# Optimization experiments

Measured on AMD Instinct MI355X. Metric: run time of the kernel, lower is better.

The kernel has to match this reference:

```python
import jax, jax.numpy as jnp
import numpy as np

B, T, C_IN, DIM, NFFT, HOP = 8, 1024, 256, 512, 1024, 256
NOUT = NFFT // 2 + 1
BB_DIL = (1, 1, 2, 2, 4, 4, 8, 8)
RES_DIL = (1, 3, 5)
N_RES = 3


def conv1d(x, w, b, dilation=1, groups=1, padding=0):
    # x: (B,C,T), w: (O, I/groups, K)
    y = jax.lax.conv_general_dilated(
        x, w, window_strides=(1,), padding=[(padding, padding)],
        rhs_dilation=(dilation,), dimension_numbers=('NCH', 'OIH', 'NCH'),
        feature_group_count=groups)
    return y + b[None, :, None]


def layernorm(x, g, b, eps=1e-6):
    m = jnp.mean(x, -1, keepdims=True)
    v = jnp.mean((x - m) ** 2, -1, keepdims=True)
    return (x - m) * jax.lax.rsqrt(v + eps) * g + b


def istft(spec, window):
    # spec: (B, F, Tf) complex, center=True, hann window, win_length=n_fft
    Bsz, F_, Tf = spec.shape
    frames = jnp.fft.irfft(spec, n=NFFT, axis=1)            # (B, n_fft, Tf)
    frames = jnp.transpose(frames, (0, 2, 1)) * window       # (B, Tf, n_fft)
    L = NFFT + HOP * (Tf - 1)
    idx = jnp.arange(Tf)[:, None] * HOP + jnp.arange(NFFT)[None, :]  # (Tf, n_fft)
    y = jnp.zeros((Bsz, L), frames.dtype).at[:, idx].add(frames)
    env = jnp.zeros((L,), window.dtype).at[idx].add(
        jnp.broadcast_to(window ** 2, (Tf, NFFT)))
    y = y / jnp.where(env > 1e-11, env, 1.0)
    start = NFFT // 2
    return y[:, start:start + HOP * (Tf - 1)]


def setup_inputs() -> dict:
    key = jax.random.key(0)
    ks = iter(jax.random.split(key, 64))
    r = lambda *s: jax.random.normal(next(ks), s, jnp.float32) * 0.02
    return {
        'x': jax.random.normal(next(ks), (B, T, C_IN), jnp.float32),
        'conv_in_w': r(DIM, C_IN, 7), 'conv_in_b': r(DIM),
        'skip_w': r(DIM, C_IN, 1), 'skip_b': r(DIM),
        'bb_dw_w': r(8, DIM, 1, 7), 'bb_dw_b': r(8, DIM),
        'bb_ln_g': jnp.ones((8, DIM), jnp.float32), 'bb_ln_b': jnp.zeros((8, DIM), jnp.float32),
        'bb_pw1_w': r(8, 4 * DIM, DIM), 'bb_pw1_b': r(8, 4 * DIM),
        'bb_pw2_w': r(8, DIM, 4 * DIM), 'bb_pw2_b': r(8, DIM),
        'bb_gamma': jnp.full((8, DIM), 1e-6, jnp.float32),
        'res_w1': r(N_RES, 3, DIM, DIM, 3), 'res_b1': r(N_RES, 3, DIM),
        'res_w2': r(N_RES, 3, DIM, DIM, 3), 'res_b2': r(N_RES, 3, DIM),
        'ln_g': jnp.ones((DIM,), jnp.float32), 'ln_b': jnp.zeros((DIM,), jnp.float32),
        'mag_w1': r(DIM, DIM), 'mag_b1': r(DIM),
        'mag_w2': r(NOUT, DIM), 'mag_b2': r(NOUT),
        'ph_w': r(NOUT, DIM), 'ph_b': r(NOUT),
        'cumsum_w': jnp.linspace(0.05, 0.4, NOUT, dtype=jnp.float32)[None, :],
        'window': (0.5 - 0.5 * jnp.cos(2.0 * jnp.pi * jnp.arange(NFFT) / NFFT)).astype(jnp.float32),
    }


def reference(x, conv_in_w, conv_in_b, skip_w, skip_b,
              bb_dw_w, bb_dw_b, bb_ln_g, bb_ln_b,
              bb_pw1_w, bb_pw1_b, bb_pw2_w, bb_pw2_b, bb_gamma,
              res_w1, res_b1, res_w2, res_b2,
              ln_g, ln_b, mag_w1, mag_b1, mag_w2, mag_b2,
              ph_w, ph_b, cumsum_w, window):
    # (B,T,C) -> (B,C,T)
    h = jnp.transpose(x, (0, 2, 1))
    skip = conv1d(h, skip_w, skip_b)                     # (B,DIM,T)
    hp = jnp.pad(h, ((0, 0), (0, 0), (3, 3)), mode='reflect')
    h = conv1d(hp, conv_in_w, conv_in_b)                 # kernel 7, pad 0 -> (B,DIM,T)
    # ConvNeXt backbone
    for i, d in enumerate(BB_DIL):
        res = h
        pad = (7 + (d - 1) * 6) // 2
        y = conv1d(h, bb_dw_w[i], bb_dw_b[i], dilation=d, groups=DIM, padding=pad)
        y = jnp.transpose(y, (0, 2, 1))                  # (B,T,DIM)
        y = layernorm(y, bb_ln_g[i], bb_ln_b[i])
        y = jax.nn.gelu(y @ bb_pw1_w[i].T + bb_pw1_b[i], approximate=False)
        y = y @ bb_pw2_w[i].T + bb_pw2_b[i]
        y = bb_gamma[i] * y
        h = res + jnp.transpose(y, (0, 2, 1))
    h = h + skip                                         # same length T
    # Residual dilated conv stacks
    for i in range(N_RES):
        for j, d in enumerate(RES_DIL):
            y = conv1d(h, res_w1[i, j], res_b1[i, j], dilation=d, padding=d)
            y = jax.nn.leaky_relu(y, 0.1)
            y = conv1d(y, res_w2[i, j], res_b2[i, j], padding=1)
            h = h + y
    h = jnp.transpose(h, (0, 2, 1))                      # (B,T,DIM)
    h = layernorm(h, ln_g, ln_b)
    # magnitude head
    m = jax.nn.gelu(h @ mag_w1.T + mag_b1, approximate=False)
    log_mag = m @ mag_w2.T + mag_b2
    mag = jnp.exp(jnp.clip(log_mag, -10.0, 10.0))        # (B,T,NOUT)
    # instantaneous-frequency phase head
    inst = jnp.tanh(h @ ph_w.T + ph_b) * jnp.pi
    phase = jnp.cumsum(inst * cumsum_w, axis=1)
    phase = jnp.remainder(phase + jnp.pi, 2.0 * jnp.pi) - jnp.pi
    # synthesize
    spec = jax.lax.complex(mag * jnp.cos(phase), mag * jnp.sin(phase))
    spec = jnp.transpose(spec, (0, 2, 1))                # (B,F,T)
    return istft(spec, window)
```

## Files before the change

### kernel.cpp

```cpp
#include <hip/hip_runtime.h>
#include <math.h>

constexpr int Bv = 8, Tv = 1024, DIMC = 512, NOUTC = 513;
constexpr int Mrows = Bv * 1024;
constexpr int LDS_S = 1056;
constexpr float PI_F = 3.14159265358979323846f;
constexpr float TWOPI_F = 6.28318530717958647692f;

struct TapInfo { int n; int off[7]; };
struct PtrTable { _Float16* h[36]; };

enum { BND_NONE = 0, BND_ZERO, BND_REFLECT };

typedef _Float16 half8v __attribute__((ext_vector_type(8)));
typedef _Float16 half4v __attribute__((ext_vector_type(4)));
typedef float f32x4 __attribute__((ext_vector_type(4)));

__device__ __forceinline__ void gld_lds16(const void* g, void* l) {
  __builtin_amdgcn_global_load_lds(
      (const __attribute__((address_space(1))) unsigned int*)g,
      (__attribute__((address_space(3))) unsigned int*)l, 16, 0, 0);
}

enum { MEPI_GELU_H = 0, MEPI_GAMMARES };

template<int EPI, int TN>
__global__ __launch_bounds__(256)
void mfma_gemm(const _Float16* __restrict__ A, int lda,
               const _Float16* __restrict__ W, int K,
               const float* __restrict__ bias,
               const float* __restrict__ aux,
               float* __restrict__ hio,
               _Float16* __restrict__ Ch,
               int N, int ldc)
{
  constexpr int NFR = TN / 32;
  __shared__ _Float16 sA[2][128 * 32];
  __shared__ _Float16 sB[2][TN * 32];
  const int m0 = blockIdx.x * 128;
  const int n0 = blockIdx.y * TN;
  const int tid = threadIdx.x;
  const int wid = tid >> 6, lane = tid & 63;
  const int wr = wid >> 1, wc = wid & 1;
  const int fr = lane & 15, fq = lane >> 4;

  f32x4 acc[4][NFR] = {};

  const int rbase = tid >> 2;
  const int kwS = (((tid & 3) ^ ((tid >> 3) & 3)) << 3);
  const int nkc = K >> 5;
  const int fqS = fq ^ ((fr >> 1) & 3);
  const int aBase = (wr * 64 + fr) * 32 + fqS * 8;
  const int bBase = (wc * (TN / 2) + fr) * 32 + fqS * 8;

  const _Float16* arow[2];
  #pragma unroll
  for (int s = 0; s < 2; ++s)
    arow[s] = A + (size_t)(m0 + s * 64 + rbase) * lda + kwS;

  auto STAGE = [&](int kc, int buf) {
    const int k0 = kc << 5;
    #pragma unroll
    for (int s = 0; s < 2; ++s)
      gld_lds16(arow[s] + k0, (char*)&sA[buf][0] + s * 4096 + wid * 1024);
    #pragma unroll
    for (int s = 0; s < TN / 64; ++s) {
      size_t bo = (size_t)(n0 + s * 64 + rbase) * K + kwS + k0;
      gld_lds16(W + bo, (char*)&sB[buf][0] + s * 4096 + wid * 1024);
    }
  };
  auto COMPUTE = [&](int buf) {
    half8v aF[4], bF[NFR];
    #pragma unroll
    for (int i = 0; i < 4; ++i) aF[i] = *(const half8v*)&sA[buf][aBase + i * 512];
    #pragma unroll
    for (int j = 0; j < NFR; ++j) bF[j] = *(const half8v*)&sB[buf][bBase + j * 512];
    #pragma unroll
    for (int i = 0; i < 4; ++i)
      #pragma unroll
      for (int j = 0; j < NFR; ++j)
        acc[i][j] = __builtin_amdgcn_mfma_f32_16x16x32_f16(aF[i], bF[j], acc[i][j], 0, 0, 0);
  };

  STAGE(0, 0);
  __syncthreads();
  int cur = 0;
  for (int kc = 0; kc < nkc; ++kc) {
    if (kc + 1 < nkc) STAGE(kc + 1, cur ^ 1);
    COMPUTE(cur);
    __syncthreads();
    cur ^= 1;
  }

  #pragma unroll
  for (int j = 0; j < NFR; ++j) {
    const int n = n0 + wc * (TN / 2) + j * 16 + fr;
    const float bj = bias[n];
    const float gj = (EPI == MEPI_GAMMARES) ? aux[n] : 0.f;
    #pragma unroll
    for (int i = 0; i < 4; ++i) {
      const int mB = m0 + wr * 64 + i * 16 + fq * 4;
      #pragma unroll
      for (int r = 0; r < 4; ++r) {
        const int m = mB + r;
        float v = acc[i][j][r] + bj;
        if (EPI == MEPI_GELU_H) {
          v = 0.5f * v * (1.f + erff(v * 0.70710678118654752f));
          Ch[(size_t)m * ldc + n] = (_Float16)v;
        } else {
          hio[(size_t)m * ldc + n] += gj * v;
        }
      }
    }
  }
}

enum { SEPI_F32 = 0, SEPI_LEAKY_SPLIT, SEPI_ADDRES_SPLIT,
       SEPI_GELU_SPLIT, SEPI_EXPCLIP, SEPI_TANHCW };

template<int EPI, int BND, int TN>
__global__ __launch_bounds__(256)
void mfma_gemm_split(const _Float16* __restrict__ Ah, const _Float16* __restrict__ Al, int lda,
                     const _Float16* __restrict__ Wh, const _Float16* __restrict__ Wl, int K,
                     const float* __restrict__ bias,
                     const float* __restrict__ aux,
                     float* __restrict__ hio,
                     float* __restrict__ Cf,
                     _Float16* __restrict__ Chh, _Float16* __restrict__ Chl,
                     int N, int ldc,
                     const _Float16* __restrict__ zpage,
                     TapInfo taps)
{
  constexpr int NFR = TN / 32;
  __shared__ _Float16 sAh[2][128 * 32];
  __shared__ _Float16 sAl[2][128 * 32];
  __shared__ _Float16 sBh[2][TN * 32];
  __shared__ _Float16 sBl[2][TN * 32];
  const int m0 = blockIdx.x * 128;
  const int n0 = blockIdx.y * TN;
  const int tid = threadIdx.x;
  const int wid = tid >> 6, lane = tid & 63;
  const int wr = wid >> 1, wc = wid & 1;
  const int fr = lane & 15, fq = lane >> 4;

  f32x4 acc[4][NFR] = {};

  const int t0 = m0 & (Tv - 1);
  const int rbase = tid >> 2;
  const int kwS = (((tid & 3) ^ ((tid >> 3) & 3)) << 3);
  const int nkc = K >> 5;
  const int NT = taps.n * nkc;
  const int fqS = fq ^ ((fr >> 1) & 3);
  const int aBase = (wr * 64 + fr) * 32 + fqS * 8;
  const int bBase = (wc * (TN / 2) + fr) * 32 + fqS * 8;

  auto STAGE = [&](int st, int buf) {
    int tap = (taps.n == 1) ? 0 : (st / nkc);
    int kc = st - tap * nkc;
    const int k0 = kc << 5;
    const int off = (BND == BND_NONE) ? 0 : taps.off[tap];
    const _Float16* Wth = Wh + (size_t)tap * N * K;
    const _Float16* Wtl = Wl + (size_t)tap * N * K;
    #pragma unroll
    for (int s = 0; s < 2; ++s) {
      int t = t0 + s * 64 + rbase + off;
      bool valid = true;
      if (BND == BND_REFLECT) t = (t < 0) ? -t : (t >= Tv ? 2 * Tv - 2 - t : t);
      else if (BND == BND_ZERO) valid = (t >= 0) && (t < Tv);
      size_t ro = (size_t)(m0 - t0 + t) * lda + kwS + k0;
      const void* sh = valid ? (const void*)(Ah + ro) : (const void*)zpage;
      const void* sl = valid ? (const void*)(Al + ro) : (const void*)zpage;
      gld_lds16(sh, (char*)&sAh[buf][0] + s * 4096 + wid * 1024);
      gld_lds16(sl, (char*)&sAl[buf][0] + s * 4096 + wid * 1024);
    }
    #pragma unroll
    for (int s = 0; s < TN / 64; ++s) {
      size_t bo = (size_t)(n0 + s * 64 + rbase) * K + kwS + k0;
      gld_lds16(Wth + bo, (char*)&sBh[buf][0] + s * 4096 + wid * 1024);
      gld_lds16(Wtl + bo, (char*)&sBl[buf][0] + s * 4096 + wid * 1024);
    }
  };

  auto COMPUTE = [&](int buf) {
    half8v ah[4], al[4], bh[NFR], bl[NFR];
    #pragma unroll
    for (int i = 0; i < 4; ++i) {
      ah[i] = *(const half8v*)&sAh[buf][aBase + i * 512];
      al[i] = *(const half8v*)&sAl[buf][aBase + i * 512];
    }
    #pragma unroll
    for (int j = 0; j < NFR; ++j) {
      bh[j] = *(const half8v*)&sBh[buf][bBase + j * 512];
      bl[j] = *(const half8v*)&sBl[buf][bBase + j * 512];
    }
    #pragma unroll
    for (int i = 0; i < 4; ++i)
      #pragma unroll
      for (int j = 0; j < NFR; ++j) {
        acc[i][j] = __builtin_amdgcn_mfma_f32_16x16x32_f16(ah[i], bh[j], acc[i][j], 0, 0, 0);
        acc[i][j] = __builtin_amdgcn_mfma_f32_16x16x32_f16(ah[i], bl[j], acc[i][j], 0, 0, 0);
        acc[i][j] = __builtin_amdgcn_mfma_f32_16x16x32_f16(al[i], bh[j], acc[i][j], 0, 0, 0);
      }
  };

  STAGE(0, 0);
  __syncthreads();
  int cur = 0;
  for (int st = 0; st < NT; ++st) {
    if (st + 1 < NT) STAGE(st + 1, cur ^ 1);
    COMPUTE(cur);
    __syncthreads();
    cur ^= 1;
  }

  #pragma unroll
  for (int j = 0; j < NFR; ++j) {
    const int n = n0 + wc * (TN / 2) + j * 16 + fr;
    const bool nok = (n < N);
    const float bj = (nok && bias) ? bias[n] : 0.f;
    const float ax = (EPI == SEPI_TANHCW && nok) ? aux[n] : 0.f;
    #pragma unroll
    for (int i = 0; i < 4; ++i) {
      const int mB = m0 + wr * 64 + i * 16 + fq * 4;
      #pragma unroll
      for (int r = 0; r < 4; ++r) {
        const int m = mB + r;
        float v = acc[i][j][r] + bj;
        if (!nok) continue;
        if (EPI == SEPI_F32) {
          Cf[(size_t)m * ldc + n] = v;
        } else if (EPI == SEPI_GELU_SPLIT) {
          v = 0.5f * v * (1.f + erff(v * 0.70710678118654752f));
          _Float16 hi = (_Float16)v;
          Chh[(size_t)m * ldc + n] = hi;
          Chl[(size_t)m * ldc + n] = (_Float16)(v - (float)hi);
        } else if (EPI == SEPI_EXPCLIP) {
          Cf[(size_t)m * ldc + n] = expf(fminf(fmaxf(v, -10.f), 10.f));
        } else if (EPI == SEPI_TANHCW) {
          Cf[(size_t)m * ldc + n] = tanhf(v) * PI_F * ax;
        }
      }
    }
  }
}

enum { REPI_LEAKY = 0, REPI_ADDRES };

template<int EPI>
__global__ __launch_bounds__(256)
void res_gemm(const _Float16* __restrict__ Ah, const _Float16* __restrict__ Al,
              const _Float16* __restrict__ Wh, const _Float16* __restrict__ Wl,
              const float* __restrict__ bias,
              float* __restrict__ hio,
              _Float16* __restrict__ Chh, _Float16* __restrict__ Chl,
              const _Float16* __restrict__ zpage,
              int d)
{
  __shared__ _Float16 sAh_[160 * 32];
  __shared__ _Float16 sAl_[160 * 32];
  __shared__ _Float16 sB_[3 * 2 * 64 * 32];
  const int m0 = blockIdx.x * 128;
  const int n0 = blockIdx.y * 64;
  const int tid = threadIdx.x;
  const int wid = tid >> 6, lane = tid & 63;
  const int wr = wid >> 1, wc = wid & 1;
  const int fr = lane & 15, fq = lane >> 4;
  const int t0 = m0 & (Tv - 1);

  f32x4 acc[4][2] = {};
  const int offs[3] = {-d, 0, d};

  for (int kc = 0; kc < 16; ++kc) {
    const int k0h = kc << 5;
    #pragma unroll
    for (int it = 0; it < 5; ++it) {
      int cb = it * 4 + wid;
      int half = (cb >= 10) ? 1 : 0;
      int rb = (cb - half * 10) * 16;
      int row = rb + (lane >> 2);
      int slot_g = (lane & 3) ^ ((row >> 1) & 3);
      int t = t0 - 16 + row;
      bool valid = (t >= 0) && (t < Tv);
      const _Float16* srcb = half ? Al : Ah;
      const void* src = valid
          ? (const void*)(srcb + (size_t)(m0 - t0 + t) * DIMC + k0h + slot_g * 8)
          : (const void*)(zpage + slot_g * 8);
      void* dst = (char*)(half ? sAl_ : sAh_) + rb * 64;
      gld_lds16(src, dst);
    }
    #pragma unroll
    for (int it = 0; it < 6; ++it) {
      int cb = it * 4 + wid;
      int tap = cb >> 3;
      int r2 = cb & 7;
      int half = r2 >> 2;
      int rb = (r2 & 3) * 16;
      int row = rb + (lane >> 2);
      int slot_g = (lane & 3) ^ ((row >> 1) & 3);
      const _Float16* srcb = (half ? Wl : Wh) + (size_t)tap * 512 * 512
                           + (size_t)(n0 + row) * 512 + k0h + slot_g * 8;
      void* dst = (char*)sB_ + ((size_t)(tap * 2 + half) * 64 + rb) * 64;
      gld_lds16(srcb, dst);
    }
    __syncthreads();

    #pragma unroll
    for (int tap = 0; tap < 3; ++tap) {
      const int off = offs[tap];
      half8v ah[4], al[4], bh[2], bl[2];
      #pragma unroll
      for (int i = 0; i < 4; ++i) {
        int rA = wr * 64 + i * 16 + fr + off + 16;
        int ab = rA * 64 + ((fq ^ ((rA >> 1) & 3)) * 16);
        ah[i] = *(const half8v*)((const char*)sAh_ + ab);
        al[i] = *(const half8v*)((const char*)sAl_ + ab);
      }
      #pragma unroll
      for (int j = 0; j < 2; ++j) {
        int rB = wc * 32 + j * 16 + fr;
        int bb = rB * 64 + ((fq ^ ((rB >> 1) & 3)) * 16);
        bh[j] = *(const half8v*)((const char*)sB_ + (tap * 2 + 0) * 4096 + bb);
        bl[j] = *(const half8v*)((const char*)sB_ + (tap * 2 + 1) * 4096 + bb);
      }
      #pragma unroll
      for (int i = 0; i < 4; ++i)
        #pragma unroll
        for (int j = 0; j < 2; ++j) {
          acc[i][j] = __builtin_amdgcn_mfma_f32_16x16x32_f16(ah[i], bh[j], acc[i][j], 0, 0, 0);
          acc[i][j] = __builtin_amdgcn_mfma_f32_16x16x32_f16(ah[i], bl[j], acc[i][j], 0, 0, 0);
          acc[i][j] = __builtin_amdgcn_mfma_f32_16x16x32_f16(al[i], bh[j], acc[i][j], 0, 0, 0);
        }
    }
    __syncthreads();
  }

  #pragma unroll
  for (int j = 0; j < 2; ++j) {
    const int n = n0 + wc * 32 + j * 16 + fr;
    const float bj = bias[n];
    #pragma unroll
    for (int i = 0; i < 4; ++i) {
      const int mB = m0 + wr * 64 + i * 16 + fq * 4;
      #pragma unroll
      for (int r = 0; r < 4; ++r) {
        const int m = mB + r;
        float v = acc[i][j][r] + bj;
        if (EPI == REPI_LEAKY) {
          v = (v > 0.f) ? v : 0.1f * v;
          _Float16 hi = (_Float16)v;
          Chh[(size_t)m * DIMC + n] = hi;
          Chl[(size_t)m * DIMC + n] = (_Float16)(v - (float)hi);
        } else {
          float nh = hio[(size_t)m * DIMC + n] + v;
          hio[(size_t)m * DIMC + n] = nh;
          _Float16 hi = (_Float16)nh;
          Chh[(size_t)m * DIMC + n] = hi;
          Chl[(size_t)m * DIMC + n] = (_Float16)(nh - (float)hi);
        }
      }
    }
  }
}

__global__ __launch_bounds__(256)
void convin_gemm(const _Float16* __restrict__ Ah, const _Float16* __restrict__ Al,
                 const _Float16* __restrict__ Wh, const _Float16* __restrict__ Wl,
                 const float* __restrict__ bias,
                 float* __restrict__ Cf)
{
  __shared__ _Float16 sAh_[160 * 32];
  __shared__ _Float16 sAl_[160 * 32];
  __shared__ _Float16 sB_[7 * 2 * 64 * 32];
  const int m0 = blockIdx.x * 128;
  const int n0 = blockIdx.y * 64;
  const int tid = threadIdx.x;
  const int wid = tid >> 6, lane = tid & 63;
  const int wr = wid >> 1, wc = wid & 1;
  const int fr = lane & 15, fq = lane >> 4;
  const int t0 = m0 & (Tv - 1);

  f32x4 acc[4][2] = {};

  for (int kc = 0; kc < 8; ++kc) {
    const int k0h = kc << 5;
    #pragma unroll
    for (int it = 0; it < 5; ++it) {
      int cb = it * 4 + wid;
      int half = (cb >= 10) ? 1 : 0;
      int rb = (cb - half * 10) * 16;
      int row = rb + (lane >> 2);
      int slot_g = (lane & 3) ^ ((row >> 1) & 3);
      int t = t0 - 16 + row;
      t = (t < 0) ? -t : (t >= Tv ? 2 * Tv - 2 - t : t);
      const _Float16* srcb = half ? Al : Ah;
      const void* src = srcb + (size_t)(m0 - t0 + t) * 256 + k0h + slot_g * 8;
      void* dst = (char*)(half ? sAl_ : sAh_) + rb * 64;
      gld_lds16(src, dst);
    }
    #pragma unroll
    for (int it = 0; it < 14; ++it) {
      int cb = it * 4 + wid;
      int tap = cb >> 3;
      int r2 = cb & 7;
      int half = r2 >> 2;
      int rb = (r2 & 3) * 16;
      int row = rb + (lane >> 2);
      int slot_g = (lane & 3) ^ ((row >> 1) & 3);
      const _Float16* srcb = (half ? Wl : Wh) + (size_t)tap * 512 * 256
                           + (size_t)(n0 + row) * 256 + k0h + slot_g * 8;
      void* dst = (char*)sB_ + ((size_t)(tap * 2 + half) * 64 + rb) * 64;
      gld_lds16(srcb, dst);
    }
    __syncthreads();

    #pragma unroll
    for (int tap = 0; tap < 7; ++tap) {
      const int off = tap - 3;
      half8v ah[4], al[4], bh[2], bl[2];
      #pragma unroll
      for (int i = 0; i < 4; ++i) {
        int rA = wr * 64 + i * 16 + fr + off + 16;
        int ab = rA * 64 + ((fq ^ ((rA >> 1) & 3)) * 16);
        ah[i] = *(const half8v*)((const char*)sAh_ + ab);
        al[i] = *(const half8v*)((const char*)sAl_ + ab);
      }
      #pragma unroll
      for (int j = 0; j < 2; ++j) {
        int rB = wc * 32 + j * 16 + fr;
        int bb = rB * 64 + ((fq ^ ((rB >> 1) & 3)) * 16);
        bh[j] = *(const half8v*)((const char*)sB_ + (tap * 2 + 0) * 4096 + bb);
        bl[j] = *(const half8v*)((const char*)sB_ + (tap * 2 + 1) * 4096 + bb);
      }
      #pragma unroll
      for (int i = 0; i < 4; ++i)
        #pragma unroll
        for (int j = 0; j < 2; ++j) {
          acc[i][j] = __builtin_amdgcn_mfma_f32_16x16x32_f16(ah[i], bh[j], acc[i][j], 0, 0, 0);
          acc[i][j] = __builtin_amdgcn_mfma_f32_16x16x32_f16(ah[i], bl[j], acc[i][j], 0, 0, 0);
          acc[i][j] = __builtin_amdgcn_mfma_f32_16x16x32_f16(al[i], bh[j], acc[i][j], 0, 0, 0);
        }
    }
    __syncthreads();
  }

  #pragma unroll
  for (int j = 0; j < 2; ++j) {
    const int n = n0 + wc * 32 + j * 16 + fr;
    const float bj = bias[n];
    #pragma unroll
    for (int i = 0; i < 4; ++i) {
      const int mB = m0 + wr * 64 + i * 16 + fq * 4;
      #pragma unroll
      for (int r = 0; r < 4; ++r) {
        const int m = mB + r;
        Cf[(size_t)m * DIMC + n] = acc[i][j][r] + bj;
      }
    }
  }
}

__global__ __launch_bounds__(256)
void dwln(const float* __restrict__ h, const float* __restrict__ wt,
          const float* __restrict__ bias, const float* __restrict__ g,
          const float* __restrict__ be, _Float16* __restrict__ out, int d)
{
  int wid = threadIdx.x >> 6, lane = threadIdx.x & 63;
  int m = (blockIdx.x << 2) + wid;
  int t = m & (Tv - 1);
  int bT = m - t;
  int c0 = lane * 8;
  float acc[8];
  {
    float4 b0 = *(const float4*)&bias[c0];
    float4 b1 = *(const float4*)&bias[c0 + 4];
    acc[0] = b0.x; acc[1] = b0.y; acc[2] = b0.z; acc[3] = b0.w;
    acc[4] = b1.x; acc[5] = b1.y; acc[6] = b1.z; acc[7] = b1.w;
  }
  #pragma unroll
  for (int k = 0; k < 7; ++k) {
    int tt = t + (k - 3) * d;
    if (tt < 0 || tt >= Tv) continue;
    const float* hp = &h[(size_t)(bT + tt) * DIMC + c0];
    float4 v0 = *(const float4*)hp;
    float4 v1 = *(const float4*)(hp + 4);
    const float* wp = &wt[k * DIMC + c0];
    float4 w0 = *(const float4*)wp;
    float4 w1 = *(const float4*)(wp + 4);
    float hv[8] = {v0.x, v0.y, v0.z, v0.w, v1.x, v1.y, v1.z, v1.w};
    float wv[8] = {w0.x, w0.y, w0.z, w0.w, w1.x, w1.y, w1.z, w1.w};
    #pragma unroll
    for (int q = 0; q < 8; ++q)
      acc[q] = fmaf(hv[q], wv[q], acc[q]);
  }
  float sum = 0.f;
  #pragma unroll
  for (int q = 0; q < 8; ++q) sum += acc[q];
  #pragma unroll
  for (int o = 32; o > 0; o >>= 1) sum += __shfl_xor(sum, o);
  float mean = sum * (1.f / 512.f);
  float vs = 0.f;
  #pragma unroll
  for (int q = 0; q < 8; ++q) { float dd = acc[q] - mean; vs = fmaf(dd, dd, vs); }
  #pragma unroll
  for (int o = 32; o > 0; o >>= 1) vs += __shfl_xor(vs, o);
  float rstd = rsqrtf(vs * (1.f / 512.f) + 1e-6f);
  float4 g0 = *(const float4*)&g[c0];
  float4 g1 = *(const float4*)&g[c0 + 4];
  float4 e0 = *(const float4*)&be[c0];
  float4 e1 = *(const float4*)&be[c0 + 4];
  float gv[8] = {g0.x, g0.y, g0.z, g0.w, g1.x, g1.y, g1.z, g1.w};
  float ev[8] = {e0.x, e0.y, e0.z, e0.w, e1.x, e1.y, e1.z, e1.w};
  half8v ov;
  #pragma unroll
  for (int q = 0; q < 8; ++q)
    ov[q] = (_Float16)((acc[q] - mean) * rstd * gv[q] + ev[q]);
  *(half8v*)&out[(size_t)m * DIMC + c0] = ov;
}

__global__ __launch_bounds__(256)
void repack_dw(const float* __restrict__ in, float* __restrict__ out)
{
  int idx = blockIdx.x * 256 + threadIdx.x;
  if (idx >= 8 * 512 * 7) return;
  int l = idx / 3584;
  int r = idx - l * 3584;
  int c = r / 7, k = r - c * 7;
  out[l * 3584 + k * 512 + c] = in[idx];
}

__global__ __launch_bounds__(256)
void lnorm_split(const float* __restrict__ in, const float* __restrict__ g,
                 const float* __restrict__ be,
                 _Float16* __restrict__ ohi, _Float16* __restrict__ olo)
{
  int wid = threadIdx.x >> 6, lane = threadIdx.x & 63;
  int m = (blockIdx.x << 2) + wid;
  int c0 = lane * 8;
  const float* row = in + (size_t)m * DIMC + c0;
  float4 v0 = *(const float4*)row;
  float4 v1 = *(const float4*)(row + 4);
  float acc[8] = {v0.x, v0.y, v0.z, v0.w, v1.x, v1.y, v1.z, v1.w};
  float sum = 0.f;
  #pragma unroll
  for (int q = 0; q < 8; ++q) sum += acc[q];
  #pragma unroll
  for (int o = 32; o > 0; o >>= 1) sum += __shfl_xor(sum, o);
  float mean = sum * (1.f / 512.f);
  float vs = 0.f;
  #pragma unroll
  for (int q = 0; q < 8; ++q) { float dd = acc[q] - mean; vs = fmaf(dd, dd, vs); }
  #pragma unroll
  for (int o = 32; o > 0; o >>= 1) vs += __shfl_xor(vs, o);
  float rstd = rsqrtf(vs * (1.f / 512.f) + 1e-6f);
  float4 g0 = *(const float4*)&g[c0];
  float4 g1 = *(const float4*)&g[c0 + 4];
  float4 e0 = *(const float4*)&be[c0];
  float4 e1 = *(const float4*)&be[c0 + 4];
  float gv[8] = {g0.x, g0.y, g0.z, g0.w, g1.x, g1.y, g1.z, g1.w};
  float ev[8] = {e0.x, e0.y, e0.z, e0.w, e1.x, e1.y, e1.z, e1.w};
  half8v hv, lv;
  #pragma unroll
  for (int q = 0; q < 8; ++q) {
    float v = (acc[q] - mean) * rstd * gv[q] + ev[q];
    _Float16 hi = (_Float16)v;
    hv[q] = hi; lv[q] = (_Float16)(v - (float)hi);
  }
  *(half8v*)&ohi[(size_t)m * DIMC + c0] = hv;
  *(half8v*)&olo[(size_t)m * DIMC + c0] = lv;
}

__global__ __launch_bounds__(256)
void add_split(float* __restrict__ a, const float* __restrict__ b,
               _Float16* __restrict__ hi, _Float16* __restrict__ lo, int n)
{
  int i = (blockIdx.x * 256 + threadIdx.x) * 4;
  if (i >= n) return;
  float4 va = *(const float4*)&a[i];
  float4 vb = *(const float4*)&b[i];
  float v[4] = {va.x + vb.x, va.y + vb.y, va.z + vb.z, va.w + vb.w};
  *(float4*)&a[i] = make_float4(v[0], v[1], v[2], v[3]);
  half4v h, l;
  #pragma unroll
  for (int q = 0; q < 4; ++q) {
    _Float16 hh = (_Float16)v[q];
    h[q] = hh; l[q] = (_Float16)(v[q] - (float)hh);
  }
  *(half4v*)&hi[i] = h;
  *(half4v*)&lo[i] = l;
}

__global__ __launch_bounds__(256)
void cvt_split(const float* __restrict__ in, _Float16* __restrict__ hi,
               _Float16* __restrict__ lo, int n)
{
  int i = (blockIdx.x * 256 + threadIdx.x) * 4;
  if (i >= n) return;
  float4 vv = *(const float4*)&in[i];
  float v[4] = {vv.x, vv.y, vv.z, vv.w};
  half4v h, l;
  #pragma unroll
  for (int q = 0; q < 4; ++q) {
    _Float16 hh = (_Float16)v[q];
    h[q] = hh; l[q] = (_Float16)(v[q] - (float)hh);
  }
  *(half4v*)&hi[i] = h;
  *(half4v*)&lo[i] = l;
}

__global__ __launch_bounds__(256)
void cvt_split_pad(const float* __restrict__ in, _Float16* __restrict__ hi,
                   _Float16* __restrict__ lo, int rows, int cols, int padRows)
{
  int i = blockIdx.x * 256 + threadIdx.x;
  if (i >= padRows * cols) return;
  int r = i / cols;
  float v = (r < rows) ? in[i] : 0.f;
  _Float16 h = (_Float16)v;
  hi[i] = h; lo[i] = (_Float16)(v - (float)h);
}

__global__ __launch_bounds__(256)
void cvt_h(const float* __restrict__ in, _Float16* __restrict__ out, int n)
{
  int i = (blockIdx.x * 256 + threadIdx.x) * 4;
  if (i >= n) return;
  float4 v = *(const float4*)&in[i];
  half4v h;
  h[0] = (_Float16)v.x; h[1] = (_Float16)v.y;
  h[2] = (_Float16)v.z; h[3] = (_Float16)v.w;
  *(half4v*)&out[i] = h;
}

__global__ __launch_bounds__(256)
void repack_split(const float* __restrict__ in, _Float16* __restrict__ hi,
                  _Float16* __restrict__ lo, int O, int C, int KT)
{
  int idx = blockIdx.x * 256 + threadIdx.x;
  if (idx >= O * C) return;
  int o = idx / C, c = idx - o * C;
  for (int k = 0; k < KT; ++k) {
    float v = in[((size_t)o * C + c) * KT + k];
    _Float16 h = (_Float16)v;
    size_t dst = ((size_t)k * O + o) * C + c;
    hi[dst] = h; lo[dst] = (_Float16)(v - (float)h);
  }
}

__global__ __launch_bounds__(256)
void repack_all(const float* __restrict__ res_w1, const float* __restrict__ res_w2,
                PtrTable pt)
{
  int blk = blockIdx.x;
  int conv = blk >> 10;
  int idx = ((blk & 1023) << 8) + threadIdx.x;
  int o = idx >> 9, c = idx & 511;
  const float* src = (conv < 9) ? (res_w1 + (size_t)conv * 786432)
                                : (res_w2 + (size_t)(conv - 9) * 786432);
  _Float16* hi = pt.h[conv * 2];
  _Float16* lo = pt.h[conv * 2 + 1];
  #pragma unroll
  for (int k = 0; k < 3; ++k) {
    float v = src[((size_t)o * 512 + c) * 3 + k];
    _Float16 hh = (_Float16)v;
    size_t dst = ((size_t)k * 512 + o) * 512 + c;
    hi[dst] = hh; lo[dst] = (_Float16)(v - (float)hh);
  }
}

__global__ __launch_bounds__(256)
void zero_fill16(_Float16* __restrict__ p)
{
  int i = threadIdx.x * 8;
  #pragma unroll
  for (int q = 0; q < 8; ++q) p[i + q] = (_Float16)0.f;
}

__global__ __launch_bounds__(256)
void build_basis_split(const float* __restrict__ window,
                       _Float16* __restrict__ bhi, _Float16* __restrict__ blo)
{
  int n = blockIdx.x;
  float wn = window[n];
  const float invN = 1.f / 1024.f;
  for (int j = threadIdx.x; j < LDS_S; j += 256) {
    float coef = 0.f;
    if (j < 513) {
      int k = j;
      if (k == 0)        coef = invN;
      else if (k == 512) coef = (n & 1) ? -invN : invN;
      else {
        int r = (k * n) & 1023;
        coef = 2.f * invN * cosf(TWOPI_F * (float)r * (1.f / 1024.f));
      }
    } else if (j < 1026) {
      int k = j - 513;
      if (k != 0 && k != 512) {
        int r = (k * n) & 1023;
        coef = -2.f * invN * sinf(TWOPI_F * (float)r * (1.f / 1024.f));
      }
    }
    float v = coef * wn;
    _Float16 hi = (_Float16)v;
    bhi[(size_t)n * LDS_S + j] = hi;
    blo[(size_t)n * LDS_S + j] = (_Float16)(v - (float)hi);
  }
}

__global__ __launch_bounds__(256)
void scan_part(const float* __restrict__ dph, float* __restrict__ psum)
{
  int b = blockIdx.x, fg = blockIdx.y;
  int w = threadIdx.x >> 6, lane = threadIdx.x & 63;
  int tc = blockIdx.z * 4 + w;
  int f = fg * 64 + lane;
  if (f >= NOUTC) return;
  const float* p = dph + (size_t)(b * Tv + tc * 32) * NOUTC + f;
  float s = 0.f;
  #pragma unroll 8
  for (int j = 0; j < 32; ++j) s += p[(size_t)j * NOUTC];
  psum[((size_t)b * 32 + tc) * 520 + f] = s;
}

__global__ __launch_bounds__(256)
void scan_off(float* __restrict__ psum)
{
  int idx = blockIdx.x * 256 + threadIdx.x;
  if (idx >= 8 * NOUTC) return;
  int b = idx / NOUTC, f = idx - b * NOUTC;
  float run = 0.f;
  for (int tc = 0; tc < 32; ++tc) {
    size_t o = ((size_t)b * 32 + tc) * 520 + f;
    float v = psum[o];
    psum[o] = run;
    run += v;
  }
}

__global__ __launch_bounds__(256)
void scan_emit(const float* __restrict__ dph, const float* __restrict__ mag,
               const float* __restrict__ psum,
               _Float16* __restrict__ Shi, _Float16* __restrict__ Slo)
{
  int b = blockIdx.x, fg = blockIdx.y;
  int w = threadIdx.x >> 6, lane = threadIdx.x & 63;
  int tc = blockIdx.z * 4 + w;
  int f = fg * 64 + lane;
  if (f >= NOUTC) return;
  float run = psum[((size_t)b * 32 + tc) * 520 + f];
  const size_t base = (size_t)(b * Tv + tc * 32) * NOUTC + f;
  for (int j = 0; j < 32; ++j) {
    run += dph[base + (size_t)j * NOUTC];
    float r = fmodf(run + PI_F, TWOPI_F);
    if (r < 0.f) r += TWOPI_F;
    float wph = r - PI_F;
    float mg = mag[base + (size_t)j * NOUTC];
    float sn, cs;
    sincosf(wph, &sn, &cs);
    size_t mrow = (size_t)(b * Tv + tc * 32 + j) * LDS_S;
    float vc = mg * cs, vs2 = mg * sn;
    _Float16 hc = (_Float16)vc, hs = (_Float16)vs2;
    Shi[mrow + f] = hc;        Slo[mrow + f] = (_Float16)(vc - (float)hc);
    Shi[mrow + 513 + f] = hs;  Slo[mrow + 513 + f] = (_Float16)(vs2 - (float)hs);
  }
}

__global__ __launch_bounds__(256)
void pad_S(_Float16* __restrict__ Shi, _Float16* __restrict__ Slo)
{
  int idx = blockIdx.x * 256 + threadIdx.x;
  if (idx >= Mrows * 30) return;
  int m = idx / 30, c = 1026 + idx % 30;
  Shi[(size_t)m * LDS_S + c] = (_Float16)0.f;
  Slo[(size_t)m * LDS_S + c] = (_Float16)0.f;
}

__global__ __launch_bounds__(256)
void ola(const float* __restrict__ frames, const float* __restrict__ window,
         float* __restrict__ out)
{
  int idx = blockIdx.x * 256 + threadIdx.x;
  if (idx >= Bv * 261888) return;
  int b = idx / 261888;
  int i = idx - b * 261888;
  int l = i + 512;
  int tmax = l >> 8; if (tmax > 1023) tmax = 1023;
  int tmin = (l >= 1023) ? ((l - 1023 + 255) >> 8) : 0;
  float acc = 0.f, env = 0.f;
  for (int t = tmin; t <= tmax; ++t) {
    int n = l - (t << 8);
    acc += frames[(size_t)(b * Tv + t) * 1024 + n];
    float wv = window[n];
    env = fmaf(wv, wv, env);
  }
  out[idx] = acc / (env > 1e-11f ? env : 1.f);
}

extern "C" void kernel_launch(void* const* d_in, const int* in_sizes, int n_in,
                              void* d_out, int out_size, void* d_ws, size_t ws_size,
                              hipStream_t stream)
{
  const float* x         = (const float*)d_in[0];
  const float* conv_in_w = (const float*)d_in[1];
  const float* conv_in_b = (const float*)d_in[2];
  const float* skip_w    = (const float*)d_in[3];
  const float* skip_b    = (const float*)d_in[4];
  const float* bb_dw_w   = (const float*)d_in[5];
  const float* bb_dw_b   = (const float*)d_in[6];
  const float* bb_ln_g   = (const float*)d_in[7];
  const float* bb_ln_b   = (const float*)d_in[8];
  const float* bb_pw1_w  = (const float*)d_in[9];
  const float* bb_pw1_b  = (const float*)d_in[10];
  const float* bb_pw2_w  = (const float*)d_in[11];
  const float* bb_pw2_b  = (const float*)d_in[12];
  const float* bb_gamma  = (const float*)d_in[13];
  const float* res_w1    = (const float*)d_in[14];
  const float* res_b1    = (const float*)d_in[15];
  const float* res_w2    = (const float*)d_in[16];
  const float* res_b2    = (const float*)d_in[17];
  const float* ln_g      = (const float*)d_in[18];
  const float* ln_b      = (const float*)d_in[19];
  const float* mag_w1    = (const float*)d_in[20];
  const float* mag_b1    = (const float*)d_in[21];
  const float* mag_w2    = (const float*)d_in[22];
  const float* mag_b2    = (const float*)d_in[23];
  const float* ph_w      = (const float*)d_in[24];
  const float* ph_b      = (const float*)d_in[25];
  const float* cumsum_w  = (const float*)d_in[26];
  const float* window    = (const float*)d_in[27];
  float* out = (float*)d_out;
  float* ws  = (float*)d_ws;

  float* w_h     = ws;
  float* w_skip  = ws + 4194304;
  float* w_t4    = ws + 8388608;
  float* w_mag   = ws + 12582912;
  float* w_dph   = ws + 16785408;
  float* w_basis = ws + 20987904;
  float* w_big   = ws + 22069248;
  _Float16* t3h  = (_Float16*)w_big;
  _Float16* h_hi = (_Float16*)w_big;
  _Float16* h_lo = h_hi + 4194304;
  _Float16* y_hi = h_hi + 8388608;
  _Float16* y_lo = h_hi + 12582912;
  _Float16* Shi  = (_Float16*)w_big;
  _Float16* Slo  = Shi + 8650752;
  float* w_frames= w_h;

  _Float16* t2h  = (_Float16*)(ws + 30720000);
  _Float16* x_hi = (_Float16*)(ws + 32817152);
  _Float16* x_lo = (_Float16*)(ws + 33865728);
  _Float16* wA_hi= (_Float16*)(ws + 34914304);
  _Float16* wA_lo= (_Float16*)(ws + 35438592);
  _Float16* wB_hi= (_Float16*)(ws + 35962880);
  _Float16* wB_lo= (_Float16*)(ws + 36487168);
  _Float16* zpg  = (_Float16*)(ws + 37011456);
  float* w_psum  = ws + 37012480;
  float* w_dwT   = ws + 37145600;

  _Float16* wpw1h = (_Float16*)w_t4;
  _Float16* wpw2h = (_Float16*)w_mag;

  static const size_t slotOffF[18] = {
    8388608, 9175040, 9961472, 10747904, 11534336,
    12582912, 13369344, 14155776, 14942208, 15728640,
    16785408, 17571840, 18358272, 19144704, 19931136,
    32817152, 33603584,
    30720000
  };
  PtrTable pt;
  for (int cv = 0; cv < 18; ++cv) {
    _Float16* hi = (_Float16*)(ws + slotOffF[cv]);
    pt.h[cv * 2] = hi;
    pt.h[cv * 2 + 1] = hi + 786432;
  }

  _Float16* lshi = (_Float16*)w_skip;
  _Float16* lslo = lshi + 4194304;
  _Float16* t4hi = (_Float16*)w_t4;
  _Float16* t4lo = t4hi + 4194304;
  _Float16* m1hi = t2h;
  _Float16* m1lo = t2h + 262144;
  _Float16* m2hi = t2h + 524288;
  _Float16* m2lo = t2h + 851968;
  _Float16* phhi = t2h + 1179648;
  _Float16* phlo = t2h + 1507328;
  _Float16* bhi  = (_Float16*)w_basis;
  _Float16* blo  = bhi + 1081344;

  dim3 blk(256);
  TapInfo tp1{1, {0}};

  zero_fill16<<<dim3(1), blk, 0, stream>>>(zpg);
  cvt_split<<<dim3(8192 * 256 / 4 / 256), blk, 0, stream>>>(x, x_hi, x_lo, 8192 * 256);
  cvt_h<<<dim3(8388608 / 4 / 256), blk, 0, stream>>>(bb_pw1_w, wpw1h, 8388608);
  cvt_h<<<dim3(8388608 / 4 / 256), blk, 0, stream>>>(bb_pw2_w, wpw2h, 8388608);
  repack_dw<<<dim3(112), blk, 0, stream>>>(bb_dw_w, w_dwT);

  repack_split<<<dim3(512 * 256 / 256), blk, 0, stream>>>(conv_in_w, wA_hi, wA_lo, 512, 256, 7);
  convin_gemm<<<dim3(64, 8), blk, 0, stream>>>(
      x_hi, x_lo, wA_hi, wA_lo, conv_in_b, w_h);
  repack_split<<<dim3(512 * 256 / 256), blk, 0, stream>>>(skip_w, wB_hi, wB_lo, 512, 256, 1);
  mfma_gemm_split<SEPI_F32, BND_NONE, 64><<<dim3(64, 8), blk, 0, stream>>>(
      x_hi, x_lo, 256, wB_hi, wB_lo, 256, skip_b, nullptr, nullptr, w_skip, nullptr, nullptr,
      512, 512, zpg, tp1);

  const int dil[8] = {1, 1, 2, 2, 4, 4, 8, 8};
  for (int i = 0; i < 8; ++i) {
    dwln<<<dim3(2048), blk, 0, stream>>>(w_h, w_dwT + i * 3584, bb_dw_b + i * 512,
                                         bb_ln_g + i * 512, bb_ln_b + i * 512, t2h, dil[i]);
    mfma_gemm<MEPI_GELU_H, 128><<<dim3(64, 16), blk, 0, stream>>>(
        t2h, 512, wpw1h + (size_t)i * 2048 * 512, 512, bb_pw1_b + i * 2048,
        nullptr, nullptr, t3h, 2048, 2048);
    mfma_gemm<MEPI_GAMMARES, 64><<<dim3(64, 8), blk, 0, stream>>>(
        t3h, 2048, wpw2h + (size_t)i * 512 * 2048, 2048, bb_pw2_b + i * 512,
        bb_gamma + i * 512, w_h, nullptr, 512, 512);
  }
  add_split<<<dim3(4194304 / 4 / 256), blk, 0, stream>>>(w_h, w_skip, h_hi, h_lo, 4194304);

  repack_all<<<dim3(18 * 1024), blk, 0, stream>>>(res_w1, res_w2, pt);

  const int rdil[3] = {1, 3, 5};
  for (int i = 0; i < 3; ++i)
    for (int j = 0; j < 3; ++j) {
      int d = rdil[j];
      int idx = i * 3 + j;
      res_gemm<REPI_LEAKY><<<dim3(64, 8), blk, 0, stream>>>(
          h_hi, h_lo, pt.h[idx * 2], pt.h[idx * 2 + 1],
          res_b1 + idx * 512, nullptr, y_hi, y_lo, zpg, d);
      res_gemm<REPI_ADDRES><<<dim3(64, 8), blk, 0, stream>>>(
          y_hi, y_lo, pt.h[(9 + idx) * 2], pt.h[(9 + idx) * 2 + 1],
          res_b2 + idx * 512, w_h, h_hi, h_lo, zpg, 1);
    }

  lnorm_split<<<dim3(2048), blk, 0, stream>>>(w_h, ln_g, ln_b, lshi, lslo);

  cvt_split<<<dim3(262144 / 4 / 256), blk, 0, stream>>>(mag_w1, m1hi, m1lo, 262144);
  cvt_split_pad<<<dim3(640 * 512 / 256), blk, 0, stream>>>(mag_w2, m2hi, m2lo, 513, 512, 640);
  cvt_split_pad<<<dim3(640 * 512 / 256), blk, 0, stream>>>(ph_w, phhi, phlo, 513, 512, 640);

  mfma_gemm_split<SEPI_GELU_SPLIT, BND_NONE, 64><<<dim3(64, 8), blk, 0, stream>>>(
      lshi, lslo, 512, m1hi, m1lo, 512, mag_b1, nullptr, nullptr, nullptr,
      t4hi, t4lo, 512, 512, zpg, tp1);
  mfma_gemm_split<SEPI_EXPCLIP, BND_NONE, 64><<<dim3(64, 10), blk, 0, stream>>>(
      t4hi, t4lo, 512, m2hi, m2lo, 512, mag_b2, nullptr, nullptr, w_mag,
      nullptr, nullptr, 513, 513, zpg, tp1);
  mfma_gemm_split<SEPI_TANHCW, BND_NONE, 64><<<dim3(64, 10), blk, 0, stream>>>(
      lshi, lslo, 512, phhi, phlo, 512, ph_b, cumsum_w, nullptr, w_dph,
      nullptr, nullptr, 513, 513, zpg, tp1);

  build_basis_split<<<dim3(1024), blk, 0, stream>>>(window, bhi, blo);
  pad_S<<<dim3((Mrows * 30 + 255) / 256), blk, 0, stream>>>(Shi, Slo);
  scan_part<<<dim3(8, 9, 8), blk, 0, stream>>>(w_dph, w_psum);
  scan_off<<<dim3(17), blk, 0, stream>>>(w_psum);
  scan_emit<<<dim3(8, 9, 8), blk, 0, stream>>>(w_dph, w_mag, w_psum, Shi, Slo);
  mfma_gemm_split<SEPI_F32, BND_NONE, 128><<<dim3(64, 8), blk, 0, stream>>>(
      Shi, Slo, LDS_S, bhi, blo, LDS_S, nullptr, nullptr, nullptr, w_frames,
      nullptr, nullptr, 1024, 1024, zpg, tp1);
  ola<<<dim3((Bv * 261888 + 255) / 256), blk, 0, stream>>>(w_frames, window, out);
}
```

Before: 1.865 ms.

## Widen res_gemm N tile to 128 and deepen K staging for pw2 GEMM

The residual dilated-conv GEMM now computes a 128-column output tile per block instead of 64. This halves the grid and reuses each staged A tile (hi/lo activations with halo) across twice as many output columns, cutting redundant A loads. The pointwise-2 backbone GEMM now stages two 32-wide K chunks per barrier, halving the synchronisation count over its K=2048 loop. In exchange, register pressure and LDS use rise, and res_gemm drops to 256 blocks, which lowers occupancy and parallelism on the GPU.

```diff
diff --git a/kernel.cpp b/kernel.cpp
--- a/kernel.cpp
+++ b/kernel.cpp
@@ -24,7 +24,7 @@
 
 enum { MEPI_GELU_H = 0, MEPI_GAMMARES };
 
-template<int EPI, int TN>
+template<int EPI, int TN, int KS>
 __global__ __launch_bounds__(256)
 void mfma_gemm(const _Float16* __restrict__ A, int lda,
                const _Float16* __restrict__ W, int K,
@@ -35,8 +35,8 @@
                int N, int ldc)
 {
   constexpr int NFR = TN / 32;
-  __shared__ _Float16 sA[2][128 * 32];
-  __shared__ _Float16 sB[2][TN * 32];
+  __shared__ _Float16 sA[2][KS * 128 * 32];
+  __shared__ _Float16 sB[2][KS * TN * 32];
   const int m0 = blockIdx.x * 128;
   const int n0 = blockIdx.y * TN;
   const int tid = threadIdx.x;
@@ -48,7 +48,7 @@
 
   const int rbase = tid >> 2;
   const int kwS = (((tid & 3) ^ ((tid >> 3) & 3)) << 3);
-  const int nkc = K >> 5;
+  const int nst = K / (32 * KS);
   const int fqS = fq ^ ((fr >> 1) & 3);
   const int aBase = (wr * 64 + fr) * 32 + fqS * 8;
   const int bBase = (wc * (TN / 2) + fr) * 32 + fqS * 8;
@@ -58,35 +58,45 @@
   for (int s = 0; s < 2; ++s)
     arow[s] = A + (size_t)(m0 + s * 64 + rbase) * lda + kwS;
 
-  auto STAGE = [&](int kc, int buf) {
-    const int k0 = kc << 5;
-    #pragma unroll
-    for (int s = 0; s < 2; ++s)
-      gld_lds16(arow[s] + k0, (char*)&sA[buf][0] + s * 4096 + wid * 1024);
-    #pragma unroll
-    for (int s = 0; s < TN / 64; ++s) {
-      size_t bo = (size_t)(n0 + s * 64 + rbase) * K + kwS + k0;
-      gld_lds16(W + bo, (char*)&sB[buf][0] + s * 4096 + wid * 1024);
+  auto STAGE = [&](int st, int buf) {
+    #pragma unroll
+    for (int ks = 0; ks < KS; ++ks) {
+      const int k0 = (st * KS + ks) << 5;
+      #pragma unroll
+      for (int s = 0; s < 2; ++s)
+        gld_lds16(arow[s] + k0,
+                  (char*)&sA[buf][0] + ks * 8192 + s * 4096 + wid * 1024);
+      #pragma unroll
+      for (int s = 0; s < TN / 64; ++s) {
+        size_t bo = (size_t)(n0 + s * 64 + rbase) * K + kwS + k0;
+        gld_lds16(W + bo,
+                  (char*)&sB[buf][0] + ks * (TN * 64) + s * 4096 + wid * 1024);
+      }
     }
   };
   auto COMPUTE = [&](int buf) {
-    half8v aF[4], bF[NFR];
-    #pragma unroll
-    for (int i = 0; i < 4; ++i) aF[i] = *(const half8v*)&sA[buf][aBase + i * 512];
-    #pragma unroll
-    for (int j = 0; j < NFR; ++j) bF[j] = *(const half8v*)&sB[buf][bBase + j * 512];
-    #pragma unroll
-    for (int i = 0; i < 4; ++i)
+    #pragma unroll
+    for (int ks = 0; ks < KS; ++ks) {
+      half8v aF[4], bF[NFR];
+      #pragma unroll
+      for (int i = 0; i < 4; ++i)
+        aF[i] = *(const half8v*)&sA[buf][ks * 4096 + aBase + i * 512];
       #pragma unroll
       for (int j = 0; j < NFR; ++j)
-        acc[i][j] = __builtin_amdgcn_mfma_f32_16x16x32_f16(aF[i], bF[j], acc[i][j], 0, 0, 0);
+        bF[j] = *(const half8v*)&sB[buf][ks * (TN * 32) + bBase + j * 512];
+      #pragma unroll
+      for (int i = 0; i < 4; ++i)
+        #pragma unroll
+        for (int j = 0; j < NFR; ++j)
+          acc[i][j] = __builtin_amdgcn_mfma_f32_16x16x32_f16(aF[i], bF[j], acc[i][j], 0, 0, 0);
+    }
   };
 
   STAGE(0, 0);
   __syncthreads();
   int cur = 0;
-  for (int kc = 0; kc < nkc; ++kc) {
-    if (kc + 1 < nkc) STAGE(kc + 1, cur ^ 1);
+  for (int st = 0; st < nst; ++st) {
+    if (st + 1 < nst) STAGE(st + 1, cur ^ 1);
     COMPUTE(cur);
     __syncthreads();
     cur ^= 1;
@@ -258,16 +268,16 @@
 {
   __shared__ _Float16 sAh_[160 * 32];
   __shared__ _Float16 sAl_[160 * 32];
-  __shared__ _Float16 sB_[3 * 2 * 64 * 32];
+  __shared__ _Float16 sB_[3 * 2 * 128 * 32];
   const int m0 = blockIdx.x * 128;
-  const int n0 = blockIdx.y * 64;
+  const int n0 = blockIdx.y * 128;
   const int tid = threadIdx.x;
   const int wid = tid >> 6, lane = tid & 63;
   const int wr = wid >> 1, wc = wid & 1;
   const int fr = lane & 15, fq = lane >> 4;
   const int t0 = m0 & (Tv - 1);
 
-  f32x4 acc[4][2] = {};
+  f32x4 acc[4][4] = {};
   const int offs[3] = {-d, 0, d};
 
   for (int kc = 0; kc < 16; ++kc) {
@@ -289,17 +299,17 @@
       gld_lds16(src, dst);
     }
     #pragma unroll
-    for (int it = 0; it < 6; ++it) {
+    for (int it = 0; it < 12; ++it) {
       int cb = it * 4 + wid;
-      int tap = cb >> 3;
-      int r2 = cb & 7;
-      int half = r2 >> 2;
-      int rb = (r2 & 3) * 16;
+      int tap = cb >> 4;
+      int r2 = cb & 15;
+      int half = r2 >> 3;
+      int rb = (r2 & 7) * 16;
       int row = rb + (lane >> 2);
       int slot_g = (lane & 3) ^ ((row >> 1) & 3);
       const _Float16* srcb = (half ? Wl : Wh) + (size_t)tap * 512 * 512
                            + (size_t)(n0 + row) * 512 + k0h + slot_g * 8;
-      void* dst = (char*)sB_ + ((size_t)(tap * 2 + half) * 64 + rb) * 64;
+      void* dst = (char*)sB_ + ((size_t)(tap * 2 + half) * 128 + rb) * 64;
       gld_lds16(srcb, dst);
     }
     __syncthreads();
@@ -307,7 +317,7 @@
     #pragma unroll
     for (int tap = 0; tap < 3; ++tap) {
       const int off = offs[tap];
-      half8v ah[4], al[4], bh[2], bl[2];
+      half8v ah[4], al[4], bh[4], bl[4];
       #pragma unroll
       for (int i = 0; i < 4; ++i) {
         int rA = wr * 64 + i * 16 + fr + off + 16;
@@ -316,16 +326,16 @@
         al[i] = *(const half8v*)((const char*)sAl_ + ab);
       }
       #pragma unroll
-      for (int j = 0; j < 2; ++j) {
-        int rB = wc * 32 + j * 16 + fr;
+      for (int j = 0; j < 4; ++j) {
+        int rB = wc * 64 + j * 16 + fr;
         int bb = rB * 64 + ((fq ^ ((rB >> 1) & 3)) * 16);
-        bh[j] = *(const half8v*)((const char*)sB_ + (tap * 2 + 0) * 4096 + bb);
-        bl[j] = *(const half8v*)((const char*)sB_ + (tap * 2 + 1) * 4096 + bb);
+        bh[j] = *(const half8v*)((const char*)sB_ + (tap * 2 + 0) * 8192 + bb);
+        bl[j] = *(const half8v*)((const char*)sB_ + (tap * 2 + 1) * 8192 + bb);
       }
       #pragma unroll
       for (int i = 0; i < 4; ++i)
         #pragma unroll
-        for (int j = 0; j < 2; ++j) {
+        for (int j = 0; j < 4; ++j) {
           acc[i][j] = __builtin_amdgcn_mfma_f32_16x16x32_f16(ah[i], bh[j], acc[i][j], 0, 0, 0);
           acc[i][j] = __builtin_amdgcn_mfma_f32_16x16x32_f16(ah[i], bl[j], acc[i][j], 0, 0, 0);
           acc[i][j] = __builtin_amdgcn_mfma_f32_16x16x32_f16(al[i], bh[j], acc[i][j], 0, 0, 0);
@@ -335,8 +345,8 @@
   }
 
   #pragma unroll
-  for (int j = 0; j < 2; ++j) {
-    const int n = n0 + wc * 32 + j * 16 + fr;
+  for (int j = 0; j < 4; ++j) {
+    const int n = n0 + wc * 64 + j * 16 + fr;
     const float bj = bias[n];
     #pragma unroll
     for (int i = 0; i < 4; ++i) {
@@ -908,10 +918,10 @@
   for (int i = 0; i < 8; ++i) {
     dwln<<<dim3(2048), blk, 0, stream>>>(w_h, w_dwT + i * 3584, bb_dw_b + i * 512,
                                          bb_ln_g + i * 512, bb_ln_b + i * 512, t2h, dil[i]);
-    mfma_gemm<MEPI_GELU_H, 128><<<dim3(64, 16), blk, 0, stream>>>(
+    mfma_gemm<MEPI_GELU_H, 128, 1><<<dim3(64, 16), blk, 0, stream>>>(
         t2h, 512, wpw1h + (size_t)i * 2048 * 512, 512, bb_pw1_b + i * 2048,
         nullptr, nullptr, t3h, 2048, 2048);
-    mfma_gemm<MEPI_GAMMARES, 64><<<dim3(64, 8), blk, 0, stream>>>(
+    mfma_gemm<MEPI_GAMMARES, 64, 2><<<dim3(64, 8), blk, 0, stream>>>(
         t3h, 2048, wpw2h + (size_t)i * 512 * 2048, 2048, bb_pw2_b + i * 512,
         bb_gamma + i * 512, w_h, nullptr, 512, 512);
   }
@@ -924,10 +934,10 @@
     for (int j = 0; j < 3; ++j) {
       int d = rdil[j];
       int idx = i * 3 + j;
-      res_gemm<REPI_LEAKY><<<dim3(64, 8), blk, 0, stream>>>(
+      res_gemm<REPI_LEAKY><<<dim3(64, 4), blk, 0, stream>>>(
           h_hi, h_lo, pt.h[idx * 2], pt.h[idx * 2 + 1],
           res_b1 + idx * 512, nullptr, y_hi, y_lo, zpg, d);
-      res_gemm<REPI_ADDRES><<<dim3(64, 8), blk, 0, stream>>>(
+      res_gemm<REPI_ADDRES><<<dim3(64, 4), blk, 0, stream>>>(
           y_hi, y_lo, pt.h[(9 + idx) * 2], pt.h[(9 + idx) * 2 + 1],
           res_b2 + idx * 512, w_h, h_hi, h_lo, zpg, 1);
     }
```

Result: slower. 2.089 ms (+12.0%).
